# Kernel tuning notes

Measured on AMD Instinct MI355X. Metric: run time of the kernel, lower is better.

## Reference

```python
import jax, jax.numpy as jnp
import numpy as np
import math

B_TOPK = 8  # self.B
NEG = -1e9  # numerically-equivalent stand-in for float('-inf') mask


def setup_inputs() -> dict:
    key = jax.random.key(0)
    ks = jax.random.split(key, 12)
    b, s, d, d_low = 4, 2048, 128, 16
    sc = 1.0 / math.sqrt(d)
    return {
        "queries": jax.random.normal(ks[0], (b, s, d), jnp.float32),
        "keys": jax.random.normal(ks[1], (b, s, d), jnp.float32),
        "values": jax.random.normal(ks[2], (b, s, d), jnp.float32),
        "valid_lens": jax.random.randint(ks[3], (b, s), 0, s, jnp.int32),
        "Wq_low": jax.random.normal(ks[4], (d, d_low), jnp.float32) * sc,
        "bq_low": jnp.zeros((d_low,), jnp.float32),
        "Wk_low": jax.random.normal(ks[5], (d, d_low), jnp.float32) * sc,
        "bk_low": jnp.zeros((d_low,), jnp.float32),
        "Wq_high": jax.random.normal(ks[6], (d, d_low), jnp.float32) * sc,
        "bq_high": jnp.zeros((d_low,), jnp.float32),
        "Wk_high": jax.random.normal(ks[7], (d, d_low), jnp.float32) * sc,
        "bk_high": jnp.zeros((d_low,), jnp.float32),
    }


def reference(queries, keys, values, valid_lens, Wq_low, bq_low, Wk_low, bk_low,
              Wq_high, bq_high, Wk_high, bk_high):
    b, s, d = queries.shape
    d_low = Wq_low.shape[1]
    scale = 1.0 / math.sqrt(d_low)

    # low-rank scores [b, sq, sk]
    q_low = queries @ Wq_low + bq_low
    k_low = keys @ Wk_low + bk_low
    scores_low = jnp.einsum('bqe,bke->bqk', q_low, k_low) * scale

    # mask: scatter -inf at (batch, valid_lens[b,k], k) along dim 1 (as in torch code)
    vl = jnp.clip(valid_lens, 0, s - 1)                      # [b, sk]
    mask = vl[:, None, :] == jnp.arange(s)[None, :, None]    # [b, sq, sk]
    scores_masked = jnp.where(mask, scores_low + NEG, scores_low)

    # top-B keys per query row (over key axis)
    _, topk_idx = jax.lax.top_k(scores_masked, B_TOPK)       # [b, s, B]

    # gather top-B queries/keys per row, project to d_low, rank-d_low correction score
    bi = jnp.arange(b)[:, None, None]
    q_high = queries[bi, topk_idx]                           # [b, s, B, d]
    k_high = keys[bi, topk_idx]                              # [b, s, B, d]
    q_proj = q_high @ Wq_high + bq_high                      # [b, s, B, d_low]
    k_proj = k_high @ Wk_high + bk_high
    score_high = jnp.sum(q_proj * k_proj, axis=-1) * scale   # [b, s, B]

    # scatter corrected scores back into the masked score matrix (dim 2)
    si = jnp.arange(s)[None, :, None]
    corrected = scores_masked.at[bi, si, topk_idx].set(score_high)

    # masked_softmax with valid_lens applies softmax over dim=1
    attn = jax.nn.softmax(corrected, axis=1)
    return jnp.einsum('bqk,bkd->bqd', attn, values)
```

## Files before the change

### kernel.cpp

```cpp
#include <hip/hip_runtime.h>
#include <float.h>
#include <math.h>

#define SEQ 2048
#define NB 4
#define DIM 128
#define DL 16
#define NEGV (-1e9f)
#define TOPK 8

#define QT 128
#define KC 64
#define QCH 64

typedef unsigned long long u64;
typedef __attribute__((ext_vector_type(8))) short short8;
typedef __attribute__((ext_vector_type(4))) float f32x4;

__device__ __forceinline__ void top8_insert(float* s, float key) {
    #pragma unroll
    for (int i = 0; i < 8; ++i) {
        float a = s[i];
        s[i] = fmaxf(a, key);
        key  = fminf(a, key);
    }
}

__device__ __forceinline__ float top8_merge16(float* s) {
    #pragma unroll
    for (int off = 1; off < 16; off <<= 1) {
        float o[8], t[8];
        #pragma unroll
        for (int i = 0; i < 8; ++i)
            o[i] = __shfl_xor(s[i], off, 64);
        #pragma unroll
        for (int i = 0; i < 8; ++i)
            t[i] = fmaxf(s[i], o[7 - i]);
        #pragma unroll
        for (int i = 0; i < 4; ++i) {
            float a = t[i], c = t[i + 4];
            t[i] = fmaxf(a, c); t[i + 4] = fminf(a, c);
        }
        #pragma unroll
        for (int g2 = 0; g2 < 8; g2 += 4) {
            float a = t[g2], c = t[g2 + 2];
            t[g2] = fmaxf(a, c); t[g2 + 2] = fminf(a, c);
            a = t[g2 + 1]; c = t[g2 + 3];
            t[g2 + 1] = fmaxf(a, c); t[g2 + 3] = fminf(a, c);
        }
        #pragma unroll
        for (int g1 = 0; g1 < 8; g1 += 2) {
            float a = t[g1], c = t[g1 + 1];
            t[g1] = fmaxf(a, c); t[g1 + 1] = fminf(a, c);
        }
        #pragma unroll
        for (int i = 0; i < 8; ++i) s[i] = t[i];
    }
    return s[7];
}

__device__ __forceinline__ unsigned bf16_rne(float x) {
    unsigned u = __float_as_uint(x);
    return (u + 0x7FFFu + ((u >> 16) & 1u)) >> 16;
}

__global__ __launch_bounds__(256) void proj_kernel(
    const float* __restrict__ q, const float* __restrict__ k,
    const float* __restrict__ Wql, const float* __restrict__ bql,
    const float* __restrict__ Wkl, const float* __restrict__ bkl,
    const float* __restrict__ Wqh, const float* __restrict__ bqh,
    const float* __restrict__ Wkh, const float* __restrict__ bkh,
    unsigned short* __restrict__ qA1, unsigned short* __restrict__ qA2,
    unsigned short* __restrict__ qA3,
    unsigned short* __restrict__ kB1, unsigned short* __restrict__ kB2,
    float* __restrict__ sh)
{
    __shared__ float Ws[4][DIM * DL];
    __shared__ float rowq[16][DIM];
    __shared__ float rowk[16][DIM];
    int tid = threadIdx.x;
    for (int i = tid; i < DIM * DL; i += 256) {
        Ws[0][i] = Wql[i];
        Ws[1][i] = Wkl[i];
        Ws[2][i] = Wqh[i];
        Ws[3][i] = Wkh[i];
    }
    int r0 = blockIdx.x * 16;
    for (int i = tid; i < 16 * DIM; i += 256) {
        int rr = i >> 7, cc = i & 127;
        rowq[rr][cc] = q[(size_t)(r0 + rr) * DIM + cc];
        rowk[rr][cc] = k[(size_t)(r0 + rr) * DIM + cc];
    }
    __syncthreads();
    int g = tid >> 4;
    int e = tid & 15;
    float aql = 0.f, akl = 0.f, aqh = 0.f, akh = 0.f;
    #pragma unroll 8
    for (int i = 0; i < DIM; ++i) {
        float qv = rowq[g][i], kv = rowk[g][i];
        aql = fmaf(qv, Ws[0][i * DL + e], aql);
        akl = fmaf(kv, Ws[1][i * DL + e], akl);
        aqh = fmaf(qv, Ws[2][i * DL + e], aqh);
        akh = fmaf(kv, Ws[3][i * DL + e], akh);
    }
    int t = r0 + g;
    float qv = aql + bql[e];
    float kv = akl + bkl[e];

    unsigned q1 = bf16_rne(qv);
    float q1f = __uint_as_float(q1 << 16);
    float qr1 = qv - q1f;
    unsigned q2 = bf16_rne(qr1);
    float q2f = __uint_as_float(q2 << 16);
    unsigned q3 = bf16_rne(qr1 - q2f);

    unsigned k1 = bf16_rne(kv);
    float k1f = __uint_as_float(k1 << 16);
    float kr1 = kv - k1f;
    unsigned k2 = bf16_rne(kr1);
    float k2f = __uint_as_float(k2 << 16);
    unsigned k3 = bf16_rne(kr1 - k2f);

    size_t pb = (size_t)t * 32;
    qA1[pb + e] = (unsigned short)q1; qA1[pb + 16 + e] = (unsigned short)q2;
    qA2[pb + e] = (unsigned short)q2; qA2[pb + 16 + e] = (unsigned short)q1;
    qA3[pb + e] = (unsigned short)q1; qA3[pb + 16 + e] = (unsigned short)q3;
    kB1[pb + e] = (unsigned short)k1; kB1[pb + 16 + e] = (unsigned short)k2;
    kB2[pb + e] = (unsigned short)k3; kB2[pb + 16 + e] = (unsigned short)k1;

    float qp = aqh + bqh[e];
    float kp = akh + bkh[e];
    float prod = qp * kp;
    #pragma unroll
    for (int off = 8; off >= 1; off >>= 1)
        prod += __shfl_xor(prod, off, 16);
    if (e == 0) sh[t] = 0.25f * prod;
}

__global__ __launch_bounds__(256) void vsplit_kernel(
    const float* __restrict__ V, unsigned short* __restrict__ VH,
    unsigned short* __restrict__ VL)
{
    __shared__ float T[32][33];
    int kb = blockIdx.x * 32, db = blockIdx.y * 32, b = blockIdx.z;
    int tid = threadIdx.x;
    {
        int r = tid >> 3, cg = tid & 7;
        float4 v = *(const float4*)(V + ((size_t)b * SEQ + kb + r) * DIM + db + cg * 4);
        T[r][cg * 4 + 0] = v.x; T[r][cg * 4 + 1] = v.y;
        T[r][cg * 4 + 2] = v.z; T[r][cg * 4 + 3] = v.w;
    }
    __syncthreads();
    int dr = tid >> 3, kg = tid & 7;
    unsigned h[4], l[4];
    #pragma unroll
    for (int j = 0; j < 4; ++j) {
        float f = T[kg * 4 + j][dr];
        unsigned hi = bf16_rne(f);
        float hf = __uint_as_float(hi << 16);
        unsigned lo = bf16_rne(f - hf);
        h[j] = hi; l[j] = lo;
    }
    size_t o = ((size_t)b * DIM + db + dr) * SEQ + kb + kg * 4;
    *(uint2*)(VH + o) = make_uint2(h[0] | (h[1] << 16), h[2] | (h[3] << 16));
    *(uint2*)(VL + o) = make_uint2(l[0] | (l[1] << 16), l[2] | (l[3] << 16));
}

__global__ __launch_bounds__(256) void score_mfma(
    const unsigned short* __restrict__ qA1, const unsigned short* __restrict__ qA2,
    const unsigned short* __restrict__ qA3,
    const unsigned short* __restrict__ kB1, const unsigned short* __restrict__ kB2,
    const int* __restrict__ valid_lens,
    float* __restrict__ Smat, float* __restrict__ thrv)
{
    __shared__ float red[4][16][8];

    int tid  = threadIdx.x;
    int lane = tid & 63;
    int wv   = tid >> 6;
    int c15  = lane & 15;
    int g    = lane >> 4;
    int row0 = __builtin_amdgcn_readfirstlane(blockIdx.x * 16);
    int b    = row0 >> 11;
    int qi0  = row0 & (SEQ - 1);

    size_t aoff = (size_t)(row0 + c15) * 32 + g * 8;
    short8 A1 = *(const short8*)(qA1 + aoff);
    short8 A2 = *(const short8*)(qA2 + aoff);
    short8 A3 = *(const short8*)(qA3 + aoff);

    const unsigned short* kb1 = kB1 + (size_t)b * SEQ * 32;
    const unsigned short* kb2 = kB2 + (size_t)b * SEQ * 32;
    const int* vlb = valid_lens + (size_t)b * SEQ;

    float s8[4][8];
    #pragma unroll
    for (int r = 0; r < 4; ++r)
        #pragma unroll
        for (int i = 0; i < 8; ++i) s8[r][i] = -FLT_MAX;

    int rowg[4];
    #pragma unroll
    for (int r = 0; r < 4; ++r) rowg[r] = qi0 + g * 4 + r;

    for (int ct = wv * 32; ct < wv * 32 + 32; ++ct) {
        int col = ct * 16 + c15;
        size_t boff = (size_t)col * 32 + g * 8;
        short8 B1 = *(const short8*)(kb1 + boff);
        short8 B2 = *(const short8*)(kb2 + boff);

        f32x4 acc = (f32x4){0.f, 0.f, 0.f, 0.f};
        acc = __builtin_amdgcn_mfma_f32_16x16x32_bf16(A1, B1, acc, 0, 0, 0);
        acc = __builtin_amdgcn_mfma_f32_16x16x32_bf16(A2, B1, acc, 0, 0, 0);
        acc = __builtin_amdgcn_mfma_f32_16x16x32_bf16(A3, B2, acc, 0, 0, 0);

        int vl = vlb[col];
        vl = vl < 0 ? 0 : (vl > SEQ - 1 ? SEQ - 1 : vl);

        float* So = Smat + (size_t)(row0 + g * 4) * SEQ + col;
        #pragma unroll
        for (int r = 0; r < 4; ++r) {
            float v = 0.25f * acc[r];
            if (vl == rowg[r]) v += NEGV;
            So[(size_t)r * SEQ] = v;
            top8_insert(s8[r], v);
        }
    }

    #pragma unroll
    for (int r = 0; r < 4; ++r) top8_merge16(s8[r]);

    if (c15 == 0) {
        #pragma unroll
        for (int r = 0; r < 4; ++r)
            #pragma unroll
            for (int i = 0; i < 8; ++i)
                red[wv][g * 4 + r][i] = s8[r][i];
    }
    __syncthreads();
    if (tid < 16) {
        float fin[8];
        #pragma unroll
        for (int i = 0; i < 8; ++i) fin[i] = red[0][tid][i];
        #pragma unroll
        for (int w2 = 1; w2 < 4; ++w2)
            #pragma unroll
            for (int i = 0; i < 8; ++i)
                top8_insert(fin, red[w2][tid][i]);
        thrv[row0 + tid] = fin[7];
    }
}

__global__ __launch_bounds__(256) void colred_partial(
    const float* __restrict__ Smat, const float* __restrict__ thrv,
    const float* __restrict__ sh,
    float* __restrict__ pm, float* __restrict__ pl)
{
    int kcol = blockIdx.x * 256 + threadIdx.x;
    int qc = blockIdx.y;
    int b  = blockIdx.z;
    const float* Sp  = Smat + (size_t)b * SEQ * SEQ + (size_t)(qc * QCH) * SEQ + kcol;
    const float* thb = thrv + (size_t)b * SEQ + qc * QCH;
    float shk = sh[(size_t)b * SEQ + kcol];
    float m = -FLT_MAX, l = 0.f;
    #pragma unroll 4
    for (int qq = 0; qq < QCH; ++qq) {
        float v = Sp[(size_t)qq * SEQ];
        float t = thb[qq];
        v = (v >= t) ? shk : v;
        float nm = fmaxf(m, v);
        l = l * __expf(m - nm) + __expf(v - nm);
        m = nm;
    }
    pm[((size_t)b * 32 + qc) * SEQ + kcol] = m;
    pl[((size_t)b * 32 + qc) * SEQ + kcol] = l;
}

__global__ __launch_bounds__(256) void colred_final(
    const float* __restrict__ pm, const float* __restrict__ pl,
    float* __restrict__ cmax, float* __restrict__ cinv)
{
    int idx = blockIdx.x * 256 + threadIdx.x;
    int b = idx >> 11, kcol = idx & (SEQ - 1);
    float m = -FLT_MAX, l = 0.f;
    #pragma unroll
    for (int c = 0; c < 32; ++c) {
        float mm = pm[((size_t)b * 32 + c) * SEQ + kcol];
        float ll = pl[((size_t)b * 32 + c) * SEQ + kcol];
        float nm = fmaxf(m, mm);
        l = l * __expf(m - nm) + ll * __expf(mm - nm);
        m = nm;
    }
    cmax[idx] = m;
    cinv[idx] = 1.f / l;
}

__global__ __launch_bounds__(256) void out_mfma(
    const float* __restrict__ Smat, const unsigned short* __restrict__ VH,
    const unsigned short* __restrict__ VL,
    const float* __restrict__ cmax, const float* __restrict__ cinv,
    const float* __restrict__ thrv, const float* __restrict__ sh,
    float* __restrict__ dst, int krange)
{
    __shared__ unsigned int VtH[DIM * 32];
    __shared__ unsigned int VtL[DIM * 32];

    int tid  = threadIdx.x;
    int w    = tid >> 6;
    int lane = tid & 63;
    int ln   = lane & 15;
    int quad = lane >> 4;
    int q0   = blockIdx.x * QT;
    int ksid = blockIdx.y;
    int b    = blockIdx.z;
    int kbeg = ksid * krange;

    const float* Sb = Smat + (size_t)b * SEQ * SEQ;
    const unsigned short* VHb = VH + (size_t)b * DIM * SEQ;
    const unsigned short* VLb = VL + (size_t)b * DIM * SEQ;
    const float* cm  = cmax + (size_t)b * SEQ;
    const float* ci  = cinv + (size_t)b * SEQ;
    const float* shb = sh + (size_t)b * SEQ;

    float thrm[2];
    #pragma unroll
    for (int mt = 0; mt < 2; ++mt)
        thrm[mt] = thrv[(size_t)b * SEQ + q0 + w * 32 + mt * 16 + ln];

    f32x4 acc[2][8];
    #pragma unroll
    for (int mt = 0; mt < 2; ++mt)
        #pragma unroll
        for (int nt = 0; nt < 8; ++nt)
            acc[mt][nt] = (f32x4){0.f, 0.f, 0.f, 0.f};

    int sd0   = tid >> 3;
    int skseg = tid & 7;

    for (int k0 = kbeg; k0 < kbeg + krange; k0 += KC) {
        #pragma unroll
        for (int it = 0; it < 4; ++it) {
            int d = sd0 + it * 32;
            size_t go = (size_t)d * SEQ + k0 + skseg * 8;
            uint4 hv = *(const uint4*)(VHb + go);
            uint4 lv = *(const uint4*)(VLb + go);
            int wa = d * 32 + ((skseg ^ (d & 7)) << 2);
            *(uint4*)&VtH[wa] = hv;
            *(uint4*)&VtL[wa] = lv;
        }

        short8 Ah[2][2], Al[2][2];
        #pragma unroll
        for (int ks = 0; ks < 2; ++ks) {
            int kk = k0 + ks * 32 + quad * 8;
            float4 cma = *(const float4*)(cm + kk);
            float4 cmb = *(const float4*)(cm + kk + 4);
            float4 cia = *(const float4*)(ci + kk);
            float4 cib = *(const float4*)(ci + kk + 4);
            float4 sha = *(const float4*)(shb + kk);
            float4 shx = *(const float4*)(shb + kk + 4);
            #pragma unroll
            for (int mt = 0; mt < 2; ++mt) {
                const float* Sp = Sb + (size_t)(q0 + w * 32 + mt * 16 + ln) * SEQ + kk;
                float4 sa = *(const float4*)Sp;
                float4 sb = *(const float4*)(Sp + 4);
                float t = thrm[mt];
                float e0 = (sa.x >= t) ? sha.x : sa.x;
                float e1 = (sa.y >= t) ? sha.y : sa.y;
                float e2 = (sa.z >= t) ? sha.z : sa.z;
                float e3 = (sa.w >= t) ? sha.w : sa.w;
                float e4 = (sb.x >= t) ? shx.x : sb.x;
                float e5 = (sb.y >= t) ? shx.y : sb.y;
                float e6 = (sb.z >= t) ? shx.z : sb.z;
                float e7 = (sb.w >= t) ? shx.w : sb.w;
                float p[8];
                p[0] = __expf(e0 - cma.x) * cia.x;
                p[1] = __expf(e1 - cma.y) * cia.y;
                p[2] = __expf(e2 - cma.z) * cia.z;
                p[3] = __expf(e3 - cma.w) * cia.w;
                p[4] = __expf(e4 - cmb.x) * cib.x;
                p[5] = __expf(e5 - cmb.y) * cib.y;
                p[6] = __expf(e6 - cmb.z) * cib.z;
                p[7] = __expf(e7 - cmb.w) * cib.w;
                #pragma unroll
                for (int j = 0; j < 8; ++j) {
                    unsigned hi = bf16_rne(p[j]);
                    float hf = __uint_as_float(hi << 16);
                    unsigned lo = bf16_rne(p[j] - hf);
                    Ah[mt][ks][j] = (short)hi;
                    Al[mt][ks][j] = (short)lo;
                }
            }
        }
        __syncthreads();

        #pragma unroll
        for (int nt = 0; nt < 8; ++nt) {
            int d = nt * 16 + ln;
            #pragma unroll
            for (int ks = 0; ks < 2; ++ks) {
                int kseg = ks * 4 + quad;
                int wa = d * 32 + ((kseg ^ (d & 7)) << 2);
                short8 bh = *(short8*)&VtH[wa];
                short8 bl = *(short8*)&VtL[wa];
                #pragma unroll
                for (int mt = 0; mt < 2; ++mt) {
                    acc[mt][nt] = __builtin_amdgcn_mfma_f32_16x16x32_bf16(
                        Ah[mt][ks], bh, acc[mt][nt], 0, 0, 0);
                    acc[mt][nt] = __builtin_amdgcn_mfma_f32_16x16x32_bf16(
                        Al[mt][ks], bh, acc[mt][nt], 0, 0, 0);
                    acc[mt][nt] = __builtin_amdgcn_mfma_f32_16x16x32_bf16(
                        Ah[mt][ks], bl, acc[mt][nt], 0, 0, 0);
                }
            }
        }
        __syncthreads();
    }

    float* dp = dst + (size_t)ksid * ((size_t)NB * SEQ * DIM)
                    + (size_t)b * SEQ * DIM;
    #pragma unroll
    for (int mt = 0; mt < 2; ++mt) {
        #pragma unroll
        for (int r = 0; r < 4; ++r) {
            float* o = dp + (size_t)(q0 + w * 32 + mt * 16 + quad * 4 + r) * DIM + ln;
            #pragma unroll
            for (int nt = 0; nt < 8; ++nt)
                o[nt * 16] = acc[mt][nt][r];
        }
    }
}

__global__ __launch_bounds__(256) void reduce_kernel(
    const float* __restrict__ part, float* __restrict__ out, int ksplit)
{
    int idx = blockIdx.x * 256 + threadIdx.x;
    const float4* p = (const float4*)part;
    float4 a = p[idx];
    for (int s = 1; s < ksplit; ++s) {
        float4 q = p[(size_t)idx + (size_t)s * 262144];
        a.x += q.x; a.y += q.y; a.z += q.z; a.w += q.w;
    }
    ((float4*)out)[idx] = a;
}

extern "C" void kernel_launch(void* const* d_in, const int* in_sizes, int n_in,
                              void* d_out, int out_size, void* d_ws, size_t ws_size,
                              hipStream_t stream)
{
    const float* queries = (const float*)d_in[0];
    const float* keys    = (const float*)d_in[1];
    const float* values  = (const float*)d_in[2];
    const int*   valid   = (const int*)d_in[3];
    const float* Wql = (const float*)d_in[4];
    const float* bql = (const float*)d_in[5];
    const float* Wkl = (const float*)d_in[6];
    const float* bkl = (const float*)d_in[7];
    const float* Wqh = (const float*)d_in[8];
    const float* bqh = (const float*)d_in[9];
    const float* Wkh = (const float*)d_in[10];
    const float* bkh = (const float*)d_in[11];

    char* ws = (char*)d_ws;
    float* Smat = (float*)(ws);
    unsigned short* qA1 = (unsigned short*)(ws + 67108864);
    unsigned short* qA2 = (unsigned short*)(ws + 67633152);
    unsigned short* qA3 = (unsigned short*)(ws + 68157440);
    unsigned short* kB1 = (unsigned short*)(ws + 68681728);
    unsigned short* kB2 = (unsigned short*)(ws + 69206016);
    float* sh    = (float*)(ws + 69730304);
    float* thrv  = (float*)(ws + 69763072);
    float* cmax  = (float*)(ws + 69795840);
    float* cinv  = (float*)(ws + 69828608);
    unsigned short* VthH = (unsigned short*)(ws + 69861376);
    unsigned short* VthL = (unsigned short*)(ws + 71958528);
    const size_t part_off = 74055680;
    float* pm    = (float*)(ws + part_off);
    float* pl    = (float*)(ws + part_off + 1048576);
    float* part  = (float*)(ws + part_off);

    const size_t part_sz  = (size_t)NB * SEQ * DIM * 4;
    int ksplit = 1;
    if      (ws_size >= part_off + 8 * part_sz) ksplit = 8;
    else if (ws_size >= part_off + 4 * part_sz) ksplit = 4;
    else if (ws_size >= part_off + 2 * part_sz) ksplit = 2;

    proj_kernel<<<dim3((NB * SEQ) / 16), 256, 0, stream>>>(
        queries, keys, Wql, bql, Wkl, bkl, Wqh, bqh, Wkh, bkh,
        qA1, qA2, qA3, kB1, kB2, sh);

    vsplit_kernel<<<dim3(SEQ / 32, DIM / 32, NB), 256, 0, stream>>>(
        values, VthH, VthL);

    score_mfma<<<dim3((NB * SEQ) / 16), 256, 0, stream>>>(
        qA1, qA2, qA3, kB1, kB2, valid, Smat, thrv);

    colred_partial<<<dim3(SEQ / 256, 32, NB), 256, 0, stream>>>(
        Smat, thrv, sh, pm, pl);

    colred_final<<<dim3((NB * SEQ) / 256), 256, 0, stream>>>(pm, pl, cmax, cinv);

    if (ksplit == 1) {
        out_mfma<<<dim3(SEQ / QT, 1, NB), 256, 0, stream>>>(
            Smat, VthH, VthL, cmax, cinv, thrv, sh, (float*)d_out, SEQ);
    } else {
        out_mfma<<<dim3(SEQ / QT, ksplit, NB), 256, 0, stream>>>(
            Smat, VthH, VthL, cmax, cinv, thrv, sh, part, SEQ / ksplit);
        reduce_kernel<<<(NB * SEQ * DIM / 4) / 256, 256, 0, stream>>>(
            part, (float*)d_out, ksplit);
    }
}
```

Measured before the change: 163.5 us.

## Fuse column softmax partial stats into score kernel epilogue

The score kernel now computes per-16-row column max/sum partials right after writing each 16-row score tile and its top-8 thresholds, while the tile is likely still in L2. This replaces the separate colred_partial pass that re-read the full 64 MB score matrix. A new final kernel reduces 128 chunk partials per column instead of 32. The trade is 4x more partial data (float2 per 16 rows), a re-read of the rows just written inside the score kernel, and extra exp work per block. It relies on row-local thresholds being final before the stats loop.

New measurement: 164.1 us, median of 2. About the same (+0.4%).

```diff
diff --git a/kernel.cpp b/kernel.cpp
--- a/kernel.cpp
+++ b/kernel.cpp
@@ -170,10 +170,12 @@
     const unsigned short* __restrict__ qA1, const unsigned short* __restrict__ qA2,
     const unsigned short* __restrict__ qA3,
     const unsigned short* __restrict__ kB1, const unsigned short* __restrict__ kB2,
-    const int* __restrict__ valid_lens,
-    float* __restrict__ Smat, float* __restrict__ thrv)
+    const int* __restrict__ valid_lens, const float* __restrict__ sh,
+    float* __restrict__ Smat, float* __restrict__ thrv,
+    float2* __restrict__ pml, int do_stats)
 {
     __shared__ float red[4][16][8];
+    __shared__ float thr_s[16];
 
     int tid  = threadIdx.x;
     int lane = tid & 63;
@@ -248,6 +250,80 @@
             for (int i = 0; i < 8; ++i)
                 top8_insert(fin, red[w2][tid][i]);
         thrv[row0 + tid] = fin[7];
+        thr_s[tid] = fin[7];
+    }
+
+    if (!do_stats) return;
+    __syncthreads();
+
+    int c0 = tid * 8;
+    const float* shb = sh + (size_t)b * SEQ;
+    float4 sh_a = *(const float4*)(shb + c0);
+    float4 sh_b = *(const float4*)(shb + c0 + 4);
+    const float* Srow = Smat + (size_t)row0 * SEQ;
+
+    float mc[8], lc[8];
+    #pragma unroll
+    for (int i = 0; i < 8; ++i) { mc[i] = -FLT_MAX; lc[i] = 0.f; }
+
+    #pragma unroll 4
+    for (int r = 0; r < 16; ++r) {
+        float t = thr_s[r];
+        float4 va = *(const float4*)(Srow + (size_t)r * SEQ + c0);
+        float4 vb = *(const float4*)(Srow + (size_t)r * SEQ + c0 + 4);
+        float e[8];
+        e[0] = (va.x >= t) ? sh_a.x : va.x;
+        e[1] = (va.y >= t) ? sh_a.y : va.y;
+        e[2] = (va.z >= t) ? sh_a.z : va.z;
+        e[3] = (va.w >= t) ? sh_a.w : va.w;
+        e[4] = (vb.x >= t) ? sh_b.x : vb.x;
+        e[5] = (vb.y >= t) ? sh_b.y : vb.y;
+        e[6] = (vb.z >= t) ? sh_b.z : vb.z;
+        e[7] = (vb.w >= t) ? sh_b.w : vb.w;
+        #pragma unroll
+        for (int i = 0; i < 8; ++i) {
+            float nm = fmaxf(mc[i], e[i]);
+            lc[i] = lc[i] * __expf(mc[i] - nm) + __expf(e[i] - nm);
+            mc[i] = nm;
+        }
+    }
+    int chunk = qi0 >> 4;
+    float2* o = pml + ((size_t)b * 128 + chunk) * SEQ + c0;
+    #pragma unroll
+    for (int i = 0; i < 8; ++i)
+        o[i] = make_float2(mc[i], lc[i]);
+}
+
+__global__ __launch_bounds__(256) void colred_final2(
+    const float2* __restrict__ pml,
+    float* __restrict__ cmax, float* __restrict__ cinv)
+{
+    __shared__ float2 red[4][64];
+    int tid = threadIdx.x;
+    int c0 = tid & 63, sl = tid >> 6;
+    int gcol = blockIdx.x * 64 + c0;
+    int b = gcol >> 11, kcol = gcol & (SEQ - 1);
+    float m = -FLT_MAX, l = 0.f;
+    #pragma unroll 8
+    for (int i = 0; i < 32; ++i) {
+        int c = sl * 32 + i;
+        float2 p = pml[((size_t)b * 128 + c) * SEQ + kcol];
+        float nm = fmaxf(m, p.x);
+        l = l * __expf(m - nm) + p.y * __expf(p.x - nm);
+        m = nm;
+    }
+    red[sl][c0] = make_float2(m, l);
+    __syncthreads();
+    if (sl == 0) {
+        #pragma unroll
+        for (int s = 1; s < 4; ++s) {
+            float2 p = red[s][c0];
+            float nm = fmaxf(m, p.x);
+            l = l * __expf(m - nm) + p.y * __expf(p.x - nm);
+            m = nm;
+        }
+        cmax[gcol] = m;
+        cinv[gcol] = 1.f / l;
     }
 }
 
@@ -475,6 +551,7 @@
     unsigned short* VthH = (unsigned short*)(ws + 69861376);
     unsigned short* VthL = (unsigned short*)(ws + 71958528);
     const size_t part_off = 74055680;
+    float2* pml  = (float2*)(ws + part_off);
     float* pm    = (float*)(ws + part_off);
     float* pl    = (float*)(ws + part_off + 1048576);
     float* part  = (float*)(ws + part_off);
@@ -485,6 +562,8 @@
     else if (ws_size >= part_off + 4 * part_sz) ksplit = 4;
     else if (ws_size >= part_off + 2 * part_sz) ksplit = 2;
 
+    int fused = (ws_size >= part_off + 8388608) ? 1 : 0;
+
     proj_kernel<<<dim3((NB * SEQ) / 16), 256, 0, stream>>>(
         queries, keys, Wql, bql, Wkl, bkl, Wqh, bqh, Wkh, bkh,
         qA1, qA2, qA3, kB1, kB2, sh);
@@ -493,12 +572,15 @@
         values, VthH, VthL);
 
     score_mfma<<<dim3((NB * SEQ) / 16), 256, 0, stream>>>(
-        qA1, qA2, qA3, kB1, kB2, valid, Smat, thrv);
-
-    colred_partial<<<dim3(SEQ / 256, 32, NB), 256, 0, stream>>>(
-        Smat, thrv, sh, pm, pl);
-
-    colred_final<<<dim3((NB * SEQ) / 256), 256, 0, stream>>>(pm, pl, cmax, cinv);
+        qA1, qA2, qA3, kB1, kB2, valid, sh, Smat, thrv, pml, fused);
+
+    if (fused) {
+        colred_final2<<<dim3((NB * SEQ) / 64), 256, 0, stream>>>(pml, cmax, cinv);
+    } else {
+        colred_partial<<<dim3(SEQ / 256, 32, NB), 256, 0, stream>>>(
+            Smat, thrv, sh, pm, pl);
+        colred_final<<<dim3((NB * SEQ) / 256), 256, 0, stream>>>(pm, pl, cmax, cinv);
+    }
 
     if (ksplit == 1) {
         out_mfma<<<dim3(SEQ / QT, 1, NB), 256, 0, stream>>>(
```
